# Performance work log

Measured on AMD Instinct MI355X. Metric: run time of the kernel, lower is better.

## Reference

```python
import jax, jax.numpy as jnp
import numpy as np

N_HEADS = 16
HEAD_DIM = 64
ROPE_BASE = 10000.0
EPS = 1e-6


def _rope_tables(T, hd, dtype):
    inv_freq = 1.0 / (ROPE_BASE ** (jnp.arange(0, hd, 2, dtype=jnp.float32) / hd))
    freqs = jnp.arange(T, dtype=jnp.float32)[:, None] * inv_freq[None, :]  # [T, hd/2]
    cos = jnp.cos(freqs)[None, :, None, :].astype(dtype)  # [1,T,1,hd/2]
    sin = jnp.sin(freqs)[None, :, None, :].astype(dtype)
    return cos, sin


def _apply_rope(x, cos, sin):
    d = x.shape[-1] // 2
    x1, x2 = x[..., :d], x[..., d:]
    return jnp.concatenate([x1 * cos + x2 * sin, -x1 * sin + x2 * cos], axis=-1)


def setup_inputs() -> dict:
    key = jax.random.key(0)
    k1, k2, k3, k4 = jax.random.split(key, 4)
    B, T, C = 4, 1024, 1024
    x = jax.random.normal(k1, (B, T, C), dtype=jnp.float32)
    W_qkv = jax.random.normal(k2, (3 * C, C), dtype=jnp.float32) * (1.0 / np.sqrt(C))
    W_out = jax.random.normal(k3, (C, C), dtype=jnp.float32) * (1.0 / np.sqrt(C))
    # learnable per-head curvature, init = exp(randn) * base_curvature (base=1.0)
    hyp_k = jnp.exp(jax.random.normal(k4, (1, N_HEADS, 1, 1), dtype=jnp.float32))
    return {"x": x, "W_qkv": W_qkv, "W_out": W_out, "hyp_k": hyp_k}


def reference(x, W_qkv, W_out, hyp_k):
    B, T, C = x.shape
    H, hd = N_HEADS, HEAD_DIM
    qkv = x @ W_qkv.T  # [B,T,3C]
    q, k, v = jnp.split(qkv, 3, axis=-1)
    q = q.reshape(B, T, H, hd)
    k = k.reshape(B, T, H, hd)
    v = v.reshape(B, T, H, hd)

    cos, sin = _rope_tables(T, hd, x.dtype)
    q = _apply_rope(q, cos, sin)
    k = _apply_rope(k, cos, sin)

    # [B,H,T,hd]
    q = q.transpose(0, 2, 1, 3)
    k = k.transpose(0, 2, 1, 3)
    v = v.transpose(0, 2, 1, 3)

    # Lorentz lift: x0 = sqrt(k + ||x||^2); inner = -x0*y0 + <x,y>;
    # dist = sqrt(k) * arccosh(-inner / k)  (geoopt Lorentz convention)
    kc = hyp_k[:, :, :, 0]  # [1,H,1]
    q0 = jnp.sqrt(kc + jnp.sum(q * q, axis=-1))  # [B,H,T]
    k0 = jnp.sqrt(kc + jnp.sum(k * k, axis=-1))  # [B,H,T]
    inner = jnp.einsum('bhld,bhsd->bhls', q, k) - q0[..., None] * k0[:, :, None, :]
    arg = jnp.maximum(-inner / hyp_k, 1.0 + EPS)
    dis = jnp.sqrt(hyp_k) * jnp.arccosh(arg)  # [B,H,L,S]

    attn_weight = 1.0 / (EPS + dis)
    causal = jnp.tril(jnp.ones((T, T), dtype=bool))
    attn_weight = jnp.where(causal, attn_weight, -jnp.inf)
    attn = jax.nn.softmax(attn_weight, axis=-1)
    out = jnp.einsum('bhls,bhsd->bhld', attn, v)  # [B,H,T,hd]
    out = out.transpose(0, 2, 1, 3).reshape(B, T, C)
    return out @ W_out.T
```

## Files before the change

kernel.cpp:

```cpp
#include <hip/hip_runtime.h>

#define B_ 4
#define T_ 1024
#define C_ 1024
#define H_ 16
#define HD_ 64

typedef short bf16x8 __attribute__((ext_vector_type(8)));
typedef float f32x4 __attribute__((ext_vector_type(4)));

__device__ __forceinline__ ushort f2bf(float f) {
    union { float f; unsigned u; } v; v.f = f;
    unsigned u = v.u;
    unsigned r = (u + 0x7fffu + ((u >> 16) & 1u)) >> 16;
    return (ushort)r;
}

__device__ __forceinline__ f32x4 mfma16(bf16x8 a, bf16x8 b, f32x4 c) {
    return __builtin_amdgcn_mfma_f32_16x16x32_bf16(a, b, c, 0, 0, 0);
}

__device__ __forceinline__ bf16x8 lds_frag(const ushort* base, int row, int byteoff) {
    int addr = (row * 128 + byteoff) ^ ((row & 7) << 4);
    uint4 u = *(const uint4*)((const char*)base + addr);
    return __builtin_bit_cast(bf16x8, u);
}

__device__ __forceinline__ bf16x8 lds_frag_v(const ushort* base, int d, int byteoff) {
    int addr = (d * 128 + byteoff) ^ ((((d & 7) ^ (d >> 3)) & 7) << 4);
    uint4 u = *(const uint4*)((const char*)base + addr);
    return __builtin_bit_cast(bf16x8, u);
}

__device__ __forceinline__ bf16x8 lds_frag_p(const ushort* base, int row, int byteoff) {
    int addr = (row * 128 + byteoff) ^ (((row >> 2) & 3) << 5);
    uint4 u = *(const uint4*)((const char*)base + addr);
    return __builtin_bit_cast(bf16x8, u);
}

__device__ __forceinline__ void bar_plain() {
    __builtin_amdgcn_sched_barrier(0);
    __builtin_amdgcn_s_barrier();
    __builtin_amdgcn_sched_barrier(0);
}
__device__ __forceinline__ void bar_lds() {
    asm volatile("s_waitcnt lgkmcnt(0)" ::: "memory");
    __builtin_amdgcn_sched_barrier(0);
    __builtin_amdgcn_s_barrier();
    __builtin_amdgcn_sched_barrier(0);
}

__global__ void cast_all(const float* __restrict__ x, const float* __restrict__ wqkv,
                         const float* __restrict__ wout,
                         ushort* __restrict__ xb, ushort* __restrict__ wqkvb,
                         ushort* __restrict__ woutb) {
    int i = (blockIdx.x * 256 + threadIdx.x) * 4;
    const float* src; ushort* dst; int off;
    if (i < 4194304)      { src = x;    dst = xb;    off = i; }
    else if (i < 7340032) { src = wqkv; dst = wqkvb; off = i - 4194304; }
    else                  { src = wout; dst = woutb; off = i - 7340032; }
    float4 v = *(const float4*)(src + off);
    ushort4 o = make_ushort4(f2bf(v.x), f2bf(v.y), f2bf(v.z), f2bf(v.w));
    *(ushort4*)(dst + off) = o;
}

#define GEMM_COMPUTE_128x64(As, Bs)                                                       \
    {                                                                                     \
        _Pragma("unroll")                                                                 \
        for (int ks = 0; ks < 2; ++ks) {                                                  \
            bf16x8 af[2], bfr[4];                                                         \
            _Pragma("unroll")                                                             \
            for (int mf = 0; mf < 2; ++mf)                                                \
                af[mf] = lds_frag(As, wv * 32 + mf * 16 + (lane & 15),                    \
                                  ks * 64 + ((lane >> 4) << 4));                          \
            _Pragma("unroll")                                                             \
            for (int nf = 0; nf < 4; ++nf)                                                \
                bfr[nf] = lds_frag(Bs, nf * 16 + (lane & 15),                             \
                                   ks * 64 + ((lane >> 4) << 4));                         \
            _Pragma("unroll")                                                             \
            for (int mf = 0; mf < 2; ++mf)                                                \
                _Pragma("unroll")                                                         \
                for (int nf = 0; nf < 4; ++nf)                                            \
                    acc[mf][nf] = mfma16(af[mf], bfr[nf], acc[mf][nf]);                   \
        }                                                                                 \
    }

#define GEMM_STAGING(Asrc, Bsrc)                                                          \
    const int srow = tid >> 3, soff = (tid & 7) * 8;                                      \
    const int swz = (srow & 7) << 4;                                                      \
    uint4 a0, a1, a2, a3, b0, b1;                                                         \
    uint4 c0, c1, c2, c3, d0, d1;                                                         \
    auto issueA = [&](int kt) {                                                           \
        const ushort* Ap = Asrc + kt * 64;                                                \
        const ushort* Bp = Bsrc + kt * 64;                                                \
        a0 = *(const uint4*)(Ap + (size_t)srow * C_ + soff);                              \
        a1 = *(const uint4*)(Ap + (size_t)(32 + srow) * C_ + soff);                       \
        a2 = *(const uint4*)(Ap + (size_t)(64 + srow) * C_ + soff);                       \
        a3 = *(const uint4*)(Ap + (size_t)(96 + srow) * C_ + soff);                       \
        b0 = *(const uint4*)(Bp + (size_t)srow * C_ + soff);                              \
        b1 = *(const uint4*)(Bp + (size_t)(32 + srow) * C_ + soff);                       \
    };                                                                                    \
    auto issueB = [&](int kt) {                                                           \
        const ushort* Ap = Asrc + kt * 64;                                                \
        const ushort* Bp = Bsrc + kt * 64;                                                \
        c0 = *(const uint4*)(Ap + (size_t)srow * C_ + soff);                              \
        c1 = *(const uint4*)(Ap + (size_t)(32 + srow) * C_ + soff);                       \
        c2 = *(const uint4*)(Ap + (size_t)(64 + srow) * C_ + soff);                       \
        c3 = *(const uint4*)(Ap + (size_t)(96 + srow) * C_ + soff);                       \
        d0 = *(const uint4*)(Bp + (size_t)srow * C_ + soff);                              \
        d1 = *(const uint4*)(Bp + (size_t)(32 + srow) * C_ + soff);                       \
    };                                                                                    \
    auto lwriteA = [&]() {                                                                \
        *(uint4*)((char*)As + ((tid * 16) ^ swz)) = a0;                                   \
        *(uint4*)((char*)As + (((tid + 256) * 16) ^ swz)) = a1;                           \
        *(uint4*)((char*)As + (((tid + 512) * 16) ^ swz)) = a2;                           \
        *(uint4*)((char*)As + (((tid + 768) * 16) ^ swz)) = a3;                           \
        *(uint4*)((char*)Bs + ((tid * 16) ^ swz)) = b0;                                   \
        *(uint4*)((char*)Bs + (((tid + 256) * 16) ^ swz)) = b1;                           \
    };                                                                                    \
    auto lwriteB = [&]() {                                                                \
        *(uint4*)((char*)As + ((tid * 16) ^ swz)) = c0;                                   \
        *(uint4*)((char*)As + (((tid + 256) * 16) ^ swz)) = c1;                           \
        *(uint4*)((char*)As + (((tid + 512) * 16) ^ swz)) = c2;                           \
        *(uint4*)((char*)As + (((tid + 768) * 16) ^ swz)) = c3;                           \
        *(uint4*)((char*)Bs + ((tid * 16) ^ swz)) = d0;                                   \
        *(uint4*)((char*)Bs + (((tid + 256) * 16) ^ swz)) = d1;                           \
    }

#define GEMM_MAIN_LOOP()                                                                  \
    issueA(0); issueB(1);                                                                 \
    for (int kt = 0; kt < 14; kt += 2) {                                                  \
        bar_plain();                                                                      \
        lwriteA();                                                                        \
        issueA(kt + 2);                                                                   \
        bar_lds();                                                                        \
        GEMM_COMPUTE_128x64(As, Bs);                                                      \
        bar_plain();                                                                      \
        lwriteB();                                                                        \
        issueB(kt + 3);                                                                   \
        bar_lds();                                                                        \
        GEMM_COMPUTE_128x64(As, Bs);                                                      \
    }                                                                                     \
    bar_plain();                                                                          \
    lwriteA();                                                                            \
    bar_lds();                                                                            \
    GEMM_COMPUTE_128x64(As, Bs);                                                          \
    bar_plain();                                                                          \
    lwriteB();                                                                            \
    bar_lds();                                                                            \
    GEMM_COMPUTE_128x64(As, Bs);

__global__ __launch_bounds__(256) void gemm_qkv(
    const ushort* __restrict__ Xb, const ushort* __restrict__ Wb,
    const float* __restrict__ hyp,
    ushort* __restrict__ Qo, ushort* __restrict__ Ko, ushort* __restrict__ Vo,
    float* __restrict__ q0g, float* __restrict__ k0g)
{
    __shared__ ushort As[128 * 64];
    __shared__ ushort Bs[64 * 64];
    const int tid = threadIdx.x, lane = tid & 63, wv = tid >> 6;
    const int m0 = blockIdx.x * 128, n0 = blockIdx.y * 64;
    const ushort* Asrc = Xb + (size_t)m0 * C_;
    const ushort* Bsrc = Wb + (size_t)n0 * C_;

    GEMM_STAGING(Asrc, Bsrc);

    f32x4 acc[2][4] = {};
    GEMM_MAIN_LOOP();

    const int sector = n0 >> 10;
    const int h = (n0 & 1023) >> 6;
    const float kc = hyp[h];
    const float inv_k = 1.0f / kc;
    float invf[2];
    invf[0] = __expf(-0.28782313662425572f * (float)(lane & 15));
    invf[1] = __expf(-0.28782313662425572f * (float)(16 + (lane & 15)));

#pragma unroll
    for (int mf = 0; mf < 2; ++mf) {
        float o[4][4];
#pragma unroll
        for (int nf = 0; nf < 4; ++nf)
#pragma unroll
            for (int r = 0; r < 4; ++r) o[nf][r] = acc[mf][nf][r];

        if (sector < 2) {
#pragma unroll
            for (int p = 0; p < 2; ++p) {
#pragma unroll
                for (int r = 0; r < 4; ++r) {
                    int m = m0 + wv * 32 + mf * 16 + ((lane >> 4) << 2) + r;
                    int t = m & (T_ - 1);
                    float sn, cs; __sincosf((float)t * invf[p], &sn, &cs);
                    float x1 = o[p][r], x2 = o[p + 2][r];
                    o[p][r]     =  x1 * cs + x2 * sn;
                    o[p + 2][r] = -x1 * sn + x2 * cs;
                }
            }
        }

#pragma unroll
        for (int r = 0; r < 4; ++r) {
            int m = m0 + wv * 32 + mf * 16 + ((lane >> 4) << 2) + r;
            int b = m >> 10, t = m & (T_ - 1);
            int bh = b * H_ + h;
            size_t base = ((size_t)bh * T_ + t) * HD_;
            float nrm = 0.f;
#pragma unroll
            for (int nf = 0; nf < 4; ++nf) {
                int d = nf * 16 + (lane & 15);
                float v = o[nf][r];
                nrm += v * v;
                ushort bv = f2bf(sector == 1 ? v * inv_k : v);
                if (sector == 0)      Qo[base + d] = bv;
                else if (sector == 1) Ko[base + d] = bv;
                else                  Vo[base + d] = bv;
            }
            if (sector < 2) {
#pragma unroll
                for (int mk = 1; mk < 16; mk <<= 1) nrm += __shfl_xor(nrm, mk);
                if ((lane & 15) == 0) {
                    float v0 = sqrtf(kc + nrm);
                    if (sector == 0) q0g[(size_t)bh * T_ + t] = v0;
                    else             k0g[(size_t)bh * T_ + t] = v0 * inv_k;
                }
            }
        }
    }
}

__global__ __launch_bounds__(256, 2) void attn_fwd(
    const ushort* __restrict__ Q, const ushort* __restrict__ K, const ushort* __restrict__ V,
    const float* __restrict__ q0g, const float* __restrict__ k0g,
    const float* __restrict__ hyp, ushort* __restrict__ AO)
{
    __shared__ ushort Ks[64 * 64];
    __shared__ ushort Vts[64 * 64];
    __shared__ ushort Ps[8][16 * 64];
    __shared__ float k0s[64];

    const int tid = threadIdx.x, lane = tid & 63, wv = tid >> 6;
    const int pr = blockIdx.x >> 6;
    const int bh = blockIdx.x & 63;
    const int h = bh & (H_ - 1);
    const int qa = pr, qb = 15 - pr, nt = qb + 1;
    const float c3 = sqrtf(hyp[h]) * 0.48045301391820142f;
    const float e3 = 6.931471805599453e-07f;

    const ushort* Kb = K + (size_t)bh * T_ * HD_;
    const ushort* Vb = V + (size_t)bh * T_ * HD_;

    bf16x8 aqA[2], aqB[2];
    {
        const ushort* qA = Q + ((size_t)bh * T_ + qa * 64 + wv * 16 + (lane & 15)) * HD_;
        const ushort* qB = Q + ((size_t)bh * T_ + qb * 64 + wv * 16 + (lane & 15)) * HD_;
#pragma unroll
        for (int ks = 0; ks < 2; ++ks) {
            aqA[ks] = __builtin_bit_cast(bf16x8, *(const uint4*)(qA + ks * 32 + ((lane >> 4) << 3)));
            aqB[ks] = __builtin_bit_cast(bf16x8, *(const uint4*)(qB + ks * 32 + ((lane >> 4) << 3)));
        }
    }
    float q0A[4], q0B[4];
#pragma unroll
    for (int r = 0; r < 4; ++r) {
        int rr = wv * 16 + ((lane >> 4) << 2) + r;
        q0A[r] = q0g[(size_t)bh * T_ + qa * 64 + rr];
        q0B[r] = q0g[(size_t)bh * T_ + qb * 64 + rr];
    }

    f32x4 oaccA[4] = {}, oaccB[4] = {};
    float lpA[4] = {}, lpB[4] = {};

    const int krow = tid >> 3, koff = tid & 7;
    const int sp = tid >> 3, dc = tid & 7;
    uint4 kv0, kv1, vv0, vv1;
    float kz = 0.f;
    auto issue = [&](int s0) {
        kv0 = *(const uint4*)(Kb + (size_t)(s0 + krow) * HD_ + koff * 8);
        kv1 = *(const uint4*)(Kb + (size_t)(s0 + 32 + krow) * HD_ + koff * 8);
        vv0 = *(const uint4*)(Vb + (size_t)(s0 + 2 * sp) * HD_ + dc * 8);
        vv1 = *(const uint4*)(Vb + (size_t)(s0 + 2 * sp + 1) * HD_ + dc * 8);
        if (tid < 64) kz = k0g[(size_t)bh * T_ + s0 + tid];
    };

    auto geom = [&](const f32x4* sc, const float* q0, const float* k0r, float p[4][4]) {
#pragma unroll
        for (int r = 0; r < 4; ++r)
#pragma unroll
            for (int sf = 0; sf < 4; ++sf) {
                float arg = fmaf(q0[r], k0r[sf], -sc[sf][r]);
                arg = fmaxf(arg, 1.0f + 1e-6f);
                float t = fmaf(arg, arg, -1.0f);
                float u = arg + __builtin_amdgcn_sqrtf(t);
                float l2 = __builtin_amdgcn_logf(u);
                float w2 = fmaf(l2, c3, e3);
                float rv = fminf(__builtin_amdgcn_rcpf(w2), 30.0f);
                p[sf][r] = __builtin_amdgcn_exp2f(rv);
            }
    };
    auto mask_diag = [&](float p[4][4]) {
        const int qloc = wv * 16 + ((lane >> 4) << 2);
#pragma unroll
        for (int r = 0; r < 4; ++r)
#pragma unroll
            for (int sf = 0; sf < 4; ++sf)
                if (sf * 16 + (lane & 15) > qloc + r) p[sf][r] = 0.f;
    };
    auto pv_step = [&](float p[4][4], ushort* ps, const bf16x8 (&vf)[2][4],
                       f32x4* oacc, float* lp) {
#pragma unroll
        for (int r = 0; r < 4; ++r) {
            int row = ((lane >> 4) << 2) + r;
#pragma unroll
            for (int sf = 0; sf < 4; ++sf) {
                int addr = (row * 128 + (sf * 16 + (lane & 15)) * 2) ^ (((row >> 2) & 3) << 5);
                *(ushort*)((char*)ps + addr) = f2bf(p[sf][r]);
            }
            lp[r] += (p[0][r] + p[1][r]) + (p[2][r] + p[3][r]);
        }
#pragma unroll
        for (int ks = 0; ks < 2; ++ks) {
            bf16x8 ap = lds_frag_p(ps, lane & 15, ks * 64 + ((lane >> 4) << 4));
#pragma unroll
            for (int df = 0; df < 4; ++df)
                oacc[df] = mfma16(ap, vf[ks][df], oacc[df]);
        }
    };

    issue(0);

    for (int it = 0; it < nt; ++it) {
        const bool actA = (it <= qa);
        __syncthreads();
        {
            *(uint4*)((char*)Ks + ((tid * 16) ^ ((krow & 7) << 4))) = kv0;
            int c1 = tid + 256;
            *(uint4*)((char*)Ks + ((c1 * 16) ^ (((c1 >> 3) & 7) << 4))) = kv1;
            union { uint4 v; ushort u[8]; } a, b;
            a.v = vv0; b.v = vv1;
#pragma unroll
            for (int j = 0; j < 8; ++j) {
                int d = dc * 8 + j;
                uint pack = (uint)a.u[j] | ((uint)b.u[j] << 16);
                *(uint*)((char*)Vts + ((d * 128 + sp * 4) ^ (((j ^ dc) & 7) << 4))) = pack;
            }
            if (tid < 64) k0s[tid] = kz;
        }
        if (it + 1 < nt) issue((it + 1) * 64);
        __syncthreads();

        bf16x8 bk[2][4];
#pragma unroll
        for (int ks = 0; ks < 2; ++ks)
#pragma unroll
            for (int sf = 0; sf < 4; ++sf)
                bk[ks][sf] = lds_frag(Ks, sf * 16 + (lane & 15), ks * 64 + ((lane >> 4) << 4));

        float k0r[4];
#pragma unroll
        for (int sf = 0; sf < 4; ++sf) k0r[sf] = k0s[sf * 16 + (lane & 15)];

        f32x4 scB[4] = {};
#pragma unroll
        for (int ks = 0; ks < 2; ++ks)
#pragma unroll
            for (int sf = 0; sf < 4; ++sf)
                scB[sf] = mfma16(aqB[ks], bk[ks][sf], scB[sf]);
        f32x4 scA[4] = {};
        if (actA) {
#pragma unroll
            for (int ks = 0; ks < 2; ++ks)
#pragma unroll
                for (int sf = 0; sf < 4; ++sf)
                    scA[sf] = mfma16(aqA[ks], bk[ks][sf], scA[sf]);
        }

        bf16x8 vf[2][4];
#pragma unroll
        for (int ks = 0; ks < 2; ++ks)
#pragma unroll
            for (int df = 0; df < 4; ++df)
                vf[ks][df] = lds_frag_v(Vts, df * 16 + (lane & 15), ks * 64 + ((lane >> 4) << 4));

        float pB[4][4];
        geom(scB, q0B, k0r, pB);
        if (it == qb) mask_diag(pB);
        pv_step(pB, Ps[wv * 2 + 1], vf, oaccB, lpB);

        if (actA) {
            float pA[4][4];
            geom(scA, q0A, k0r, pA);
            if (it == qa) mask_diag(pA);
            pv_step(pA, Ps[wv * 2 + 0], vf, oaccA, lpA);
        }
    }

    const int b = bh >> 4;
    auto epi = [&](f32x4* oacc, float* lp, int qt) {
#pragma unroll
        for (int r = 0; r < 4; ++r) {
            float s = lp[r];
#pragma unroll
            for (int mk = 1; mk < 16; mk <<= 1) s += __shfl_xor(s, mk);
            float invl = __builtin_amdgcn_rcpf(s);
            int t = qt * 64 + wv * 16 + ((lane >> 4) << 2) + r;
            size_t base = ((size_t)b * T_ + t) * C_ + h * HD_;
#pragma unroll
            for (int df = 0; df < 4; ++df)
                AO[base + df * 16 + (lane & 15)] = f2bf(oacc[df][r] * invl);
        }
    };
    epi(oaccA, lpA, qa);
    epi(oaccB, lpB, qb);
}

__global__ __launch_bounds__(256) void gemm_out(
    const ushort* __restrict__ Ab, const ushort* __restrict__ Wb, float* __restrict__ Out)
{
    __shared__ ushort As[128 * 64];
    __shared__ ushort Bs[64 * 64];
    const int tid = threadIdx.x, lane = tid & 63, wv = tid >> 6;
    const int m0 = blockIdx.x * 128, n0 = blockIdx.y * 64;
    const ushort* Asrc = Ab + (size_t)m0 * C_;
    const ushort* Bsrc = Wb + (size_t)n0 * C_;

    GEMM_STAGING(Asrc, Bsrc);

    f32x4 acc[2][4] = {};
    GEMM_MAIN_LOOP();

#pragma unroll
    for (int mf = 0; mf < 2; ++mf)
#pragma unroll
        for (int r = 0; r < 4; ++r) {
            int m = m0 + wv * 32 + mf * 16 + ((lane >> 4) << 2) + r;
#pragma unroll
            for (int nf = 0; nf < 4; ++nf) {
                int n = n0 + nf * 16 + (lane & 15);
                Out[(size_t)m * C_ + n] = acc[mf][nf][r];
            }
        }
}

extern "C" void kernel_launch(void* const* d_in, const int* in_sizes, int n_in,
                              void* d_out, int out_size, void* d_ws, size_t ws_size,
                              hipStream_t stream)
{
    const float* x    = (const float*)d_in[0];
    const float* wqkv = (const float*)d_in[1];
    const float* wout = (const float*)d_in[2];
    const float* hyp  = (const float*)d_in[3];

    char* ws = (char*)d_ws;
    ushort* xb    = (ushort*)(ws + 0);
    ushort* wqkvb = (ushort*)(ws + 8388608);
    ushort* woutb = (ushort*)(ws + 14680064);
    ushort* Qb    = (ushort*)(ws + 16777216);
    ushort* Kb    = (ushort*)(ws + 25165824);
    ushort* Vb    = (ushort*)(ws + 33554432);
    ushort* Ab    = (ushort*)(ws + 41943040);
    float*  q0    = (float*)(ws + 50331648);
    float*  k0    = (float*)(ws + 50593792);

    cast_all<<<8192, 256, 0, stream>>>(x, wqkv, wout, xb, wqkvb, woutb);

    gemm_qkv<<<dim3(32, 48), 256, 0, stream>>>(xb, wqkvb, hyp, Qb, Kb, Vb, q0, k0);
    attn_fwd<<<512, 256, 0, stream>>>(Qb, Kb, Vb, q0, k0, hyp, Ab);
    gemm_out<<<dim3(32, 16), 256, 0, stream>>>(Ab, woutb, (float*)d_out);
}
```

Measured before the change: 96.24 us.

## Double-buffer LDS tiles in both GEMMs and share attention P scratch per wave

Both GEMM kernels get two shared-memory buffers for the A/B tiles and alternate between them. The next tile is written to the idle buffer while the current one is computed, so each k-step needs one barrier instead of two. The register staging set drops from two sets of global-load registers to one. The attention kernel also reuses a single per-wave P scratch buffer for both query tiles instead of two, halving that shared allocation. The cost is doubled LDS use in the GEMMs (about 48KB per block), which may lower occupancy.

```diff
diff --git a/kernel.cpp b/kernel.cpp
--- a/kernel.cpp
+++ b/kernel.cpp
@@ -38,11 +38,6 @@
     return __builtin_bit_cast(bf16x8, u);
 }
 
-__device__ __forceinline__ void bar_plain() {
-    __builtin_amdgcn_sched_barrier(0);
-    __builtin_amdgcn_s_barrier();
-    __builtin_amdgcn_sched_barrier(0);
-}
 __device__ __forceinline__ void bar_lds() {
     asm volatile("s_waitcnt lgkmcnt(0)" ::: "memory");
     __builtin_amdgcn_sched_barrier(0);
@@ -85,12 +80,11 @@
         }                                                                                 \
     }
 
-#define GEMM_STAGING(Asrc, Bsrc)                                                          \
+#define GEMM_DBUF_STAGING(Asrc, Bsrc)                                                     \
     const int srow = tid >> 3, soff = (tid & 7) * 8;                                      \
     const int swz = (srow & 7) << 4;                                                      \
     uint4 a0, a1, a2, a3, b0, b1;                                                         \
-    uint4 c0, c1, c2, c3, d0, d1;                                                         \
-    auto issueA = [&](int kt) {                                                           \
+    auto issue = [&](int kt) {                                                            \
         const ushort* Ap = Asrc + kt * 64;                                                \
         const ushort* Bp = Bsrc + kt * 64;                                                \
         a0 = *(const uint4*)(Ap + (size_t)srow * C_ + soff);                              \
@@ -100,55 +94,42 @@
         b0 = *(const uint4*)(Bp + (size_t)srow * C_ + soff);                              \
         b1 = *(const uint4*)(Bp + (size_t)(32 + srow) * C_ + soff);                       \
     };                                                                                    \
-    auto issueB = [&](int kt) {                                                           \
-        const ushort* Ap = Asrc + kt * 64;                                                \
-        const ushort* Bp = Bsrc + kt * 64;                                                \
-        c0 = *(const uint4*)(Ap + (size_t)srow * C_ + soff);                              \
-        c1 = *(const uint4*)(Ap + (size_t)(32 + srow) * C_ + soff);                       \
-        c2 = *(const uint4*)(Ap + (size_t)(64 + srow) * C_ + soff);                       \
-        c3 = *(const uint4*)(Ap + (size_t)(96 + srow) * C_ + soff);                       \
-        d0 = *(const uint4*)(Bp + (size_t)srow * C_ + soff);                              \
-        d1 = *(const uint4*)(Bp + (size_t)(32 + srow) * C_ + soff);                       \
-    };                                                                                    \
-    auto lwriteA = [&]() {                                                                \
-        *(uint4*)((char*)As + ((tid * 16) ^ swz)) = a0;                                   \
-        *(uint4*)((char*)As + (((tid + 256) * 16) ^ swz)) = a1;                           \
-        *(uint4*)((char*)As + (((tid + 512) * 16) ^ swz)) = a2;                           \
-        *(uint4*)((char*)As + (((tid + 768) * 16) ^ swz)) = a3;                           \
-        *(uint4*)((char*)Bs + ((tid * 16) ^ swz)) = b0;                                   \
-        *(uint4*)((char*)Bs + (((tid + 256) * 16) ^ swz)) = b1;                           \
-    };                                                                                    \
-    auto lwriteB = [&]() {                                                                \
-        *(uint4*)((char*)As + ((tid * 16) ^ swz)) = c0;                                   \
-        *(uint4*)((char*)As + (((tid + 256) * 16) ^ swz)) = c1;                           \
-        *(uint4*)((char*)As + (((tid + 512) * 16) ^ swz)) = c2;                           \
-        *(uint4*)((char*)As + (((tid + 768) * 16) ^ swz)) = c3;                           \
-        *(uint4*)((char*)Bs + ((tid * 16) ^ swz)) = d0;                                   \
-        *(uint4*)((char*)Bs + (((tid + 256) * 16) ^ swz)) = d1;                           \
-    }
-
-#define GEMM_MAIN_LOOP()                                                                  \
-    issueA(0); issueB(1);                                                                 \
-    for (int kt = 0; kt < 14; kt += 2) {                                                  \
-        bar_plain();                                                                      \
-        lwriteA();                                                                        \
-        issueA(kt + 2);                                                                   \
+    auto lwrite = [&](ushort* Ad, ushort* Bd) {                                           \
+        *(uint4*)((char*)Ad + ((tid * 16) ^ swz)) = a0;                                   \
+        *(uint4*)((char*)Ad + (((tid + 256) * 16) ^ swz)) = a1;                           \
+        *(uint4*)((char*)Ad + (((tid + 512) * 16) ^ swz)) = a2;                           \
+        *(uint4*)((char*)Ad + (((tid + 768) * 16) ^ swz)) = a3;                           \
+        *(uint4*)((char*)Bd + ((tid * 16) ^ swz)) = b0;                                   \
+        *(uint4*)((char*)Bd + (((tid + 256) * 16) ^ swz)) = b1;                           \
+    }
+
+#define GEMM_DBUF_LOOP()                                                                  \
+    issue(0);                                                                             \
+    lwrite(As0, Bs0);                                                                     \
+    issue(1);                                                                             \
+    bar_lds();                                                                            \
+    for (int kt = 0; kt < 12; kt += 2) {                                                  \
+        lwrite(As1, Bs1);                                                                 \
+        issue(kt + 2);                                                                    \
+        GEMM_COMPUTE_128x64(As0, Bs0);                                                    \
         bar_lds();                                                                        \
-        GEMM_COMPUTE_128x64(As, Bs);                                                      \
-        bar_plain();                                                                      \
-        lwriteB();                                                                        \
-        issueB(kt + 3);                                                                   \
+        lwrite(As0, Bs0);                                                                 \
+        issue(kt + 3);                                                                    \
+        GEMM_COMPUTE_128x64(As1, Bs1);                                                    \
         bar_lds();                                                                        \
-        GEMM_COMPUTE_128x64(As, Bs);                                                      \
     }                                                                                     \
-    bar_plain();                                                                          \
-    lwriteA();                                                                            \
+    lwrite(As1, Bs1);                                                        \
+    issue(14);                                                                            \
+    GEMM_COMPUTE_128x64(As0, Bs0);                                           \
     bar_lds();                                                                            \
-    GEMM_COMPUTE_128x64(As, Bs);                                                          \
-    bar_plain();                                                                          \
-    lwriteB();                                                                            \
+    lwrite(As0, Bs0);                                                        \
+    issue(15);                                                                            \
+    GEMM_COMPUTE_128x64(As1, Bs1);                                           \
     bar_lds();                                                                            \
-    GEMM_COMPUTE_128x64(As, Bs);
+    lwrite(As1, Bs1);                                                        \
+    GEMM_COMPUTE_128x64(As0, Bs0);                                           \
+    bar_lds();                                                                            \
+    GEMM_COMPUTE_128x64(As1, Bs1);
 
 __global__ __launch_bounds__(256) void gemm_qkv(
     const ushort* __restrict__ Xb, const ushort* __restrict__ Wb,
@@ -156,17 +137,17 @@
     ushort* __restrict__ Qo, ushort* __restrict__ Ko, ushort* __restrict__ Vo,
     float* __restrict__ q0g, float* __restrict__ k0g)
 {
-    __shared__ ushort As[128 * 64];
-    __shared__ ushort Bs[64 * 64];
+    __shared__ ushort As0[128 * 64], Bs0[64 * 64];
+    __shared__ ushort As1[128 * 64], Bs1[64 * 64];
     const int tid = threadIdx.x, lane = tid & 63, wv = tid >> 6;
     const int m0 = blockIdx.x * 128, n0 = blockIdx.y * 64;
     const ushort* Asrc = Xb + (size_t)m0 * C_;
     const ushort* Bsrc = Wb + (size_t)n0 * C_;
 
-    GEMM_STAGING(Asrc, Bsrc);
+    GEMM_DBUF_STAGING(Asrc, Bsrc);
 
     f32x4 acc[2][4] = {};
-    GEMM_MAIN_LOOP();
+    GEMM_DBUF_LOOP();
 
     const int sector = n0 >> 10;
     const int h = (n0 & 1023) >> 6;
@@ -236,7 +217,7 @@
 {
     __shared__ ushort Ks[64 * 64];
     __shared__ ushort Vts[64 * 64];
-    __shared__ ushort Ps[8][16 * 64];
+    __shared__ ushort Ps[4][16 * 64];
     __shared__ float k0s[64];
 
     const int tid = threadIdx.x, lane = tid & 63, wv = tid >> 6;
@@ -385,13 +366,13 @@
         float pB[4][4];
         geom(scB, q0B, k0r, pB);
         if (it == qb) mask_diag(pB);
-        pv_step(pB, Ps[wv * 2 + 1], vf, oaccB, lpB);
+        pv_step(pB, Ps[wv], vf, oaccB, lpB);
 
         if (actA) {
             float pA[4][4];
             geom(scA, q0A, k0r, pA);
             if (it == qa) mask_diag(pA);
-            pv_step(pA, Ps[wv * 2 + 0], vf, oaccA, lpA);
+            pv_step(pA, Ps[wv], vf, oaccA, lpA);
         }
     }
 
@@ -417,17 +398,17 @@
 __global__ __launch_bounds__(256) void gemm_out(
     const ushort* __restrict__ Ab, const ushort* __restrict__ Wb, float* __restrict__ Out)
 {
-    __shared__ ushort As[128 * 64];
-    __shared__ ushort Bs[64 * 64];
+    __shared__ ushort As0[128 * 64], Bs0[64 * 64];
+    __shared__ ushort As1[128 * 64], Bs1[64 * 64];
     const int tid = threadIdx.x, lane = tid & 63, wv = tid >> 6;
     const int m0 = blockIdx.x * 128, n0 = blockIdx.y * 64;
     const ushort* Asrc = Ab + (size_t)m0 * C_;
     const ushort* Bsrc = Wb + (size_t)n0 * C_;
 
-    GEMM_STAGING(Asrc, Bsrc);
+    GEMM_DBUF_STAGING(Asrc, Bsrc);
 
     f32x4 acc[2][4] = {};
-    GEMM_MAIN_LOOP();
+    GEMM_DBUF_LOOP();
 
 #pragma unroll
     for (int mf = 0; mf < 2; ++mf)
```

Result: no change. 95.50 us (-0.8%).
